# Kernel optimization log

Hardware: AMD Instinct MI355X
Metric: run time of the kernel (lower is better)

## Reference

```python
import jax, jax.numpy as jnp
import numpy as np

B, N, M, DC, NUM_ITERS = 64, 1024, 512, 6, 5
# leave-one-out index table: row j lists the DC-1 positions != j
LOO = np.array([[k for k in range(DC) if k != j] for j in range(DC)])  # [DC, DC-1]


def setup_inputs() -> dict:
    key = jax.random.key(0)
    k1, k2, k3, k4 = jax.random.split(key, 4)
    rng = np.random.default_rng(0)
    # row-regular sparse parity-check matrix: each check touches exactly DC variables
    row_cols = np.stack([np.sort(rng.choice(N, DC, replace=False)) for _ in range(M)]).astype(np.int32)
    H = np.zeros((M, N), np.float32)
    H[np.arange(M)[:, None], row_cols] = 1.0
    soft_input = jax.random.normal(k1, (B, N), jnp.float32) * 2.0  # channel LLRs
    labels = jax.random.randint(k2, (B, N), 0, 2).astype(jnp.int64)
    # neural_network_process: Dense(4) then Dense(1), no bias, non-negative weights
    W1 = jnp.abs(jax.random.normal(k3, (DC - 1, 4), jnp.float32)) * 0.3
    W2 = jnp.abs(jax.random.normal(k4, (4, 1), jnp.float32)) * 0.3
    bit_w1 = jnp.full((1,), -0.048, jnp.float32)
    bit_w2 = jnp.full((1,), -0.048, jnp.float32)
    return dict(soft_input=soft_input, labels=labels, H=jnp.asarray(H),
                row_cols=jnp.asarray(row_cols), W1=W1, W2=W2,
                bit_w1=bit_w1, bit_w2=bit_w2)


def reference(soft_input, labels, H, row_cols, W1, W2, bit_w1, bit_w2):
    # NMS-r belief propagation: NUM_ITERS iterations of vc update, check-node
    # update via sorted leave-one-out magnitudes fed to a tiny non-neg NN,
    # and marginalization. Returns all soft outputs [NUM_ITERS+1, B, N].
    rows = jnp.arange(M)[:, None]                 # [M,1] for gather/scatter
    sp1 = jax.nn.softplus(bit_w1)                 # bit weight 1 (compute_vc)
    sp2 = jax.nn.softplus(bit_w2)                 # bit weight 2 (marginalize)
    loo = jnp.asarray(LOO)

    def body(cv, _):
        # compute_vc
        temp = cv.sum(axis=1) + soft_input * sp1  # [B,N]
        vc = temp[:, None, :] * H - cv            # [B,M,N]
        # compute_cv1: sign part
        s = jnp.sign((1.0 - H)[None] + vc)        # +1 at H==0 positions
        result_sign = jnp.prod(s, axis=-1)[..., None] * H * s
        # magnitude part: gather the DC nonzeros per check row
        nz = jnp.abs(vc)[:, rows, row_cols]       # [B,M,DC]
        srt = jnp.sort(nz[..., loo], axis=-1)     # [B,M,DC,DC-1] sorted ascending
        vals = ((srt @ W1) @ W2)[..., 0]          # tiny NN -> [B,M,DC]
        cv_dense = jnp.zeros_like(vc).at[:, rows, row_cols].set(vals)
        cv_new = jax.lax.stop_gradient(result_sign) * cv_dense
        # marginalize
        soft_out = cv_new.sum(axis=1) + sp2 * soft_input
        return cv_new, soft_out

    cv0 = jnp.zeros((soft_input.shape[0], M, N), jnp.float32)
    _, outs = jax.lax.scan(body, cv0, None, length=NUM_ITERS)
    return jnp.concatenate([soft_input[None], outs], axis=0)  # soft_output_list
```

## Files before the change

kernel.cpp:

```cpp
#include <hip/hip_runtime.h>


constexpr int BB    = 64;
constexpr int NCOL  = 1024;
constexpr int KDC   = 6;
constexpr int ITERS = 5;
constexpr int TOT   = BB * NCOL;
constexpr int CPL   = 8;
constexpr int JV    = 8;

__device__ __forceinline__ float softplusf(float x) {
    return fmaxf(x, 0.f) + log1pf(expf(-fabsf(x)));
}

__global__ void __launch_bounds__(64, 1) k_decode(
        const float* __restrict__ soft,
        const int*   __restrict__ row_cols,
        const float* __restrict__ W1,
        const float* __restrict__ W2,
        const float* __restrict__ bw1,
        const float* __restrict__ bw2,
        float* __restrict__ out) {
    __shared__ float S[NCOL];

    const int l = threadIdx.x;
    const int b = blockIdx.x;

    const float sp1 = softplusf(bw1[0]);
    const float sp2 = softplusf(bw2[0]);
    const float dsp = sp2 - sp1;

    float w[KDC - 1];
#pragma unroll
    for (int j = 0; j < KDC - 1; ++j) {
        float a = 0.f;
#pragma unroll
        for (int q = 0; q < 4; ++q) a += W1[j * 4 + q] * W2[q];
        w[j] = a;
    }

    float2 sv[JV];
    const float* sbp = soft + b * NCOL;
    float* ob0 = out + b * NCOL;
#pragma unroll
    for (int j = 0; j < JV; ++j) {
        const int n = 2 * l + 128 * j;
        sv[j] = *reinterpret_cast<const float2*>(sbp + n);
        *reinterpret_cast<float2*>(ob0 + n) = sv[j];
        *reinterpret_cast<float2*>(&S[n]) =
            make_float2(sp1 * sv[j].x, sp1 * sv[j].y);
    }

    int   cols[CPL * KDC];
    float cv[CPL * KDC];
    {
        const int4* rp = reinterpret_cast<const int4*>(row_cols) + 12 * l;
#pragma unroll
        for (int t = 0; t < 12; ++t) {
            const int4 q = rp[t];
            cols[4 * t]     = q.x;  cols[4 * t + 1] = q.y;
            cols[4 * t + 2] = q.z;  cols[4 * t + 3] = q.w;
        }
#pragma unroll
        for (int e = 0; e < CPL * KDC; ++e) cv[e] = 0.f;
    }
    __syncthreads();

#pragma unroll 1
    for (int p = 0; p < ITERS; ++p) {
        float v[CPL * KDC];
#pragma unroll
        for (int e = 0; e < CPL * KDC; ++e) v[e] = S[cols[e]] - cv[e];

        float2 mg[JV];
#pragma unroll
        for (int j = 0; j < JV; ++j) {
            const int n = 2 * l + 128 * j;
            mg[j] = *reinterpret_cast<const float2*>(&S[n]);
        }
        if (p >= 1) {
            float* op = out + (size_t)p * TOT + b * NCOL;
#pragma unroll
            for (int j = 0; j < JV; ++j) {
                const int n = 2 * l + 128 * j;
                *reinterpret_cast<float2*>(op + n) = make_float2(
                    fmaf(dsp, sv[j].x, mg[j].x), fmaf(dsp, sv[j].y, mg[j].y));
            }
        }
#pragma unroll
        for (int j = 0; j < JV; ++j) {
            const int n = 2 * l + 128 * j;
            *reinterpret_cast<float2*>(&S[n]) =
                make_float2(sp1 * sv[j].x, sp1 * sv[j].y);
        }

#pragma unroll
        for (int jc = 0; jc < CPL; ++jc) {
            const int e0 = jc * KDC;
#define CE(i, j) { bool sw = fabsf(v[e0+(i)]) > fabsf(v[e0+(j)]);             \
            float tv = sw ? v[e0+(j)] : v[e0+(i)];                            \
            v[e0+(j)] = sw ? v[e0+(i)] : v[e0+(j)]; v[e0+(i)] = tv;           \
            int tc = sw ? cols[e0+(j)] : cols[e0+(i)];                        \
            cols[e0+(j)] = sw ? cols[e0+(i)] : cols[e0+(j)]; cols[e0+(i)] = tc; }
            CE(0,1)
            CE(1,2) CE(0,1)
            CE(2,3) CE(1,2) CE(0,1)
            CE(3,4) CE(2,3) CE(1,2) CE(0,1)
            CE(4,5) CE(3,4) CE(2,3) CE(1,2) CE(0,1)
#undef CE
            float        mgv[KDC];
            unsigned int sb[KDC];
#pragma unroll
            for (int r = 0; r < KDC; ++r) {
                mgv[r] = fabsf(v[e0 + r]);
                sb[r]  = __float_as_uint(v[e0 + r]) & 0x80000000u;
            }
            const unsigned int Pb = sb[0] ^ sb[1] ^ sb[2] ^ sb[3] ^ sb[4] ^ sb[5];

            float pre[KDC];
            pre[0] = 0.f;
#pragma unroll
            for (int r = 0; r < KDC - 1; ++r) pre[r + 1] = pre[r] + mgv[r] * w[r];
            float suf[KDC];
            suf[KDC - 1] = 0.f;
#pragma unroll
            for (int r = KDC - 2; r >= 0; --r) suf[r] = suf[r + 1] + mgv[r + 1] * w[r];

#pragma unroll
            for (int r = 0; r < KDC; ++r) {
                const float cvn = __uint_as_float(
                    __float_as_uint(pre[r] + suf[r]) | (Pb ^ sb[r]));
                cv[e0 + r] = cvn;
                atomicAdd(&S[cols[e0 + r]], cvn);
            }
        }
        __syncthreads();
    }

    float* op = out + (size_t)ITERS * TOT + b * NCOL;
#pragma unroll
    for (int j = 0; j < JV; ++j) {
        const int n = 2 * l + 128 * j;
        const float2 t = *reinterpret_cast<const float2*>(&S[n]);
        *reinterpret_cast<float2*>(op + n) = make_float2(
            fmaf(dsp, sv[j].x, t.x), fmaf(dsp, sv[j].y, t.y));
    }
}

extern "C" void kernel_launch(void* const* d_in, const int* in_sizes, int n_in,
                              void* d_out, int out_size, void* d_ws, size_t ws_size,
                              hipStream_t stream) {
    const float* soft     = (const float*)d_in[0];
    const int*   row_cols = (const int*)d_in[3];
    const float* W1       = (const float*)d_in[4];
    const float* W2       = (const float*)d_in[5];
    const float* bw1      = (const float*)d_in[6];
    const float* bw2      = (const float*)d_in[7];
    float* out = (float*)d_out;

    k_decode<<<dim3(BB), dim3(64), 0, stream>>>(soft, row_cols, W1, W2,
                                                bw1, bw2, out);
}
```

Measured before the change: 91.43 us.

## Spread check rows over four waves with triple-buffered shared accumulators

After: 92.17 us. About the same (+0.8%).

```diff
diff --git a/kernel.cpp b/kernel.cpp
--- a/kernel.cpp
+++ b/kernel.cpp
@@ -5,15 +5,16 @@
 constexpr int NCOL  = 1024;
 constexpr int KDC   = 6;
 constexpr int ITERS = 5;
+constexpr int THR   = 256;
 constexpr int TOT   = BB * NCOL;
-constexpr int CPL   = 8;
-constexpr int JV    = 8;
+constexpr int CPL   = 2;
+constexpr int JV    = 2;
 
 __device__ __forceinline__ float softplusf(float x) {
     return fmaxf(x, 0.f) + log1pf(expf(-fabsf(x)));
 }
 
-__global__ void __launch_bounds__(64, 1) k_decode(
+__global__ void __launch_bounds__(THR, 1) k_decode(
         const float* __restrict__ soft,
         const int*   __restrict__ row_cols,
         const float* __restrict__ W1,
@@ -21,10 +22,10 @@
         const float* __restrict__ bw1,
         const float* __restrict__ bw2,
         float* __restrict__ out) {
-    __shared__ float S[NCOL];
+    __shared__ float S[3][NCOL];
 
-    const int l = threadIdx.x;
-    const int b = blockIdx.x;
+    const int tid = threadIdx.x;
+    const int b   = blockIdx.x;
 
     const float sp1 = softplusf(bw1[0]);
     const float sp2 = softplusf(bw2[0]);
@@ -44,19 +45,20 @@
     float* ob0 = out + b * NCOL;
 #pragma unroll
     for (int j = 0; j < JV; ++j) {
-        const int n = 2 * l + 128 * j;
+        const int n = 2 * tid + 512 * j;
         sv[j] = *reinterpret_cast<const float2*>(sbp + n);
         *reinterpret_cast<float2*>(ob0 + n) = sv[j];
-        *reinterpret_cast<float2*>(&S[n]) =
-            make_float2(sp1 * sv[j].x, sp1 * sv[j].y);
+        const float2 bs = make_float2(sp1 * sv[j].x, sp1 * sv[j].y);
+        *reinterpret_cast<float2*>(&S[0][n]) = bs;
+        *reinterpret_cast<float2*>(&S[1][n]) = bs;
     }
 
     int   cols[CPL * KDC];
     float cv[CPL * KDC];
     {
-        const int4* rp = reinterpret_cast<const int4*>(row_cols) + 12 * l;
+        const int4* rp = reinterpret_cast<const int4*>(row_cols) + 3 * tid;
 #pragma unroll
-        for (int t = 0; t < 12; ++t) {
+        for (int t = 0; t < 3; ++t) {
             const int4 q = rp[t];
             cols[4 * t]     = q.x;  cols[4 * t + 1] = q.y;
             cols[4 * t + 2] = q.z;  cols[4 * t + 3] = q.w;
@@ -68,30 +70,29 @@
 
 #pragma unroll 1
     for (int p = 0; p < ITERS; ++p) {
+        const int rd = p % 3, ac = (p + 1) % 3, zr = (p + 2) % 3;
+
         float v[CPL * KDC];
 #pragma unroll
-        for (int e = 0; e < CPL * KDC; ++e) v[e] = S[cols[e]] - cv[e];
+        for (int e = 0; e < CPL * KDC; ++e) v[e] = S[rd][cols[e]] - cv[e];
 
-        float2 mg[JV];
-#pragma unroll
-        for (int j = 0; j < JV; ++j) {
-            const int n = 2 * l + 128 * j;
-            mg[j] = *reinterpret_cast<const float2*>(&S[n]);
-        }
         if (p >= 1) {
             float* op = out + (size_t)p * TOT + b * NCOL;
 #pragma unroll
             for (int j = 0; j < JV; ++j) {
-                const int n = 2 * l + 128 * j;
+                const int n = 2 * tid + 512 * j;
+                const float2 t = *reinterpret_cast<const float2*>(&S[rd][n]);
                 *reinterpret_cast<float2*>(op + n) = make_float2(
-                    fmaf(dsp, sv[j].x, mg[j].x), fmaf(dsp, sv[j].y, mg[j].y));
+                    fmaf(dsp, sv[j].x, t.x), fmaf(dsp, sv[j].y, t.y));
             }
         }
+        if (p < ITERS - 1) {
 #pragma unroll
-        for (int j = 0; j < JV; ++j) {
-            const int n = 2 * l + 128 * j;
-            *reinterpret_cast<float2*>(&S[n]) =
-                make_float2(sp1 * sv[j].x, sp1 * sv[j].y);
+            for (int j = 0; j < JV; ++j) {
+                const int n = 2 * tid + 512 * j;
+                *reinterpret_cast<float2*>(&S[zr][n]) =
+                    make_float2(sp1 * sv[j].x, sp1 * sv[j].y);
+            }
         }
 
 #pragma unroll
@@ -131,7 +132,7 @@
                 const float cvn = __uint_as_float(
                     __float_as_uint(pre[r] + suf[r]) | (Pb ^ sb[r]));
                 cv[e0 + r] = cvn;
-                atomicAdd(&S[cols[e0 + r]], cvn);
+                atomicAdd(&S[ac][cols[e0 + r]], cvn);
             }
         }
         __syncthreads();
@@ -140,8 +141,8 @@
     float* op = out + (size_t)ITERS * TOT + b * NCOL;
 #pragma unroll
     for (int j = 0; j < JV; ++j) {
-        const int n = 2 * l + 128 * j;
-        const float2 t = *reinterpret_cast<const float2*>(&S[n]);
+        const int n = 2 * tid + 512 * j;
+        const float2 t = *reinterpret_cast<const float2*>(&S[ITERS % 3][n]);
         *reinterpret_cast<float2*>(op + n) = make_float2(
             fmaf(dsp, sv[j].x, t.x), fmaf(dsp, sv[j].y, t.y));
     }
@@ -158,6 +159,6 @@
     const float* bw2      = (const float*)d_in[7];
     float* out = (float*)d_out;
 
-    k_decode<<<dim3(BB), dim3(64), 0, stream>>>(soft, row_cols, W1, W2,
-                                                bw1, bw2, out);
+    k_decode<<<dim3(BB), dim3(THR), 0, stream>>>(soft, row_cols, W1, W2,
+                                                 bw1, bw2, out);
 }
```
